# Kernel tuning notes

Measured on AMD Instinct MI355X. Metric: run time of the kernel, lower is better.

The kernel has to match this reference:

```python
import jax, jax.numpy as jnp
import numpy as np

N_ANCHORS = 25
N_CLASSES = 16
X_IMG = 296
Y_IMG = 296
OPLIST = ['conv','conv','MP','conv','conv','MP','conv','conv','conv','MP','conv','conv','conv','MP','conv','conv','conv']

def _size_list(s):
    out = [s]
    for op in OPLIST:
        out.append(out[-1] - 2 if op == 'conv' else out[-1] // 2)
    return out

XLIST = _size_list(X_IMG)  # ends at 7
YLIST = _size_list(Y_IMG)
FEAT = XLIST[-1]           # final feature-map size (7)
GRID = XLIST[-1] - 2       # anchor grid (5), source's xlist[-1]-2 convention
B, C = 2, 512


def setup_inputs() -> dict:
    key = jax.random.key(0)
    ks = jax.random.split(key, 12)
    D = C * 49
    return {
        'cfeats':   jax.random.normal(ks[0], (B, C, FEAT, FEAT), jnp.float32),
        'regcls':   jax.random.normal(ks[1], (B, 5, N_ANCHORS, GRID, GRID), jnp.float32) * 0.5,
        'wanchors': jax.random.uniform(ks[2], (N_ANCHORS, GRID, GRID), jnp.float32, 16.0, 128.0),
        'hanchors': jax.random.uniform(ks[3], (N_ANCHORS, GRID, GRID), jnp.float32, 16.0, 128.0),
        'xanchors': jax.random.uniform(ks[4], (N_ANCHORS, GRID, GRID), jnp.float32, 0.0, float(X_IMG)),
        'yanchors': jax.random.uniform(ks[5], (N_ANCHORS, GRID, GRID), jnp.float32, 0.0, float(Y_IMG)),
        'w1': jax.random.normal(ks[6], (200, D), jnp.float32) * 0.02,
        'b1': jnp.zeros((200,), jnp.float32),
        'w2': jax.random.normal(ks[7], (100, 200), jnp.float32) * 0.02,
        'b2': jnp.zeros((100,), jnp.float32),
        'w3': jax.random.normal(ks[8], (N_CLASSES + 1, 100), jnp.float32) * 0.02,
        'b3': jnp.zeros((N_CLASSES + 1,), jnp.float32),
        'w4': jax.random.normal(ks[9], (4 * (N_CLASSES + 1), 100), jnp.float32) * 0.02,
        'b4': jnp.zeros((4 * (N_CLASSES + 1),), jnp.float32),
    }


def _forward(cfeats, regcls, wanchors, hanchors, xanchors, yanchors,
             w1, b1, w2, b2, w3, b3, w4, b4):
    Bq, Cq, Fq, _ = cfeats.shape
    A, G = N_ANCHORS, GRID
    # ---- anchor-box decode ----
    wreg = jnp.exp(regcls[:, 2]) * wanchors
    hreg = jnp.exp(regcls[:, 3]) * hanchors
    xreg = regcls[:, 0] * wanchors + xanchors
    yreg = regcls[:, 1] * hanchors + yanchors
    xis = xreg - wreg / 2.0
    yis = yreg - hreg / 2.0
    xfs = xreg + wreg / 2.0
    yfs = yreg + hreg / 2.0
    c0 = jnp.floor(jax.nn.relu(xis))
    c1 = jnp.floor(jax.nn.relu(yis))
    c2 = jnp.minimum(jnp.ceil(xfs), float(X_IMG - 1))
    c3 = jnp.maximum(jnp.ceil(yfs), float(Y_IMG - 1))  # (sic) max, as in source
    valid = (xis < float(X_IMG)) & (yis < float(Y_IMG)) & (xfs >= 0.0) & (yfs >= 0.0)
    c4 = jnp.where(valid, jax.nn.sigmoid(regcls[:, 4]), 0.0)
    # ---- track coords through the conv/MP stack ----
    for i, op in enumerate(OPLIST):
        if op == 'conv':
            c0 = jax.nn.relu(c0 - 1.0)
            c1 = jax.nn.relu(c1 - 1.0)
            c2 = jnp.minimum(c2, float(XLIST[i + 1] - 1))
            c3 = jnp.minimum(c3, float(YLIST[i + 1] - 1))
        else:
            c0 = jnp.floor(c0 / 2.0); c1 = jnp.floor(c1 / 2.0)
            c2 = jnp.floor(c2 / 2.0); c3 = jnp.floor(c3 / 2.0)
    N = A * G * G  # flatten (anchor, x, y) -> roi index, same order as source
    xi = c0.reshape(Bq, N).astype(jnp.int32)
    yi = c1.reshape(Bq, N).astype(jnp.int32)
    xf = c2.reshape(Bq, N).astype(jnp.int32)
    yf = c3.reshape(Bq, N).astype(jnp.int32)
    roi_on = c4.reshape(Bq, N) > 0.0
    # ---- 7x7 RoIPool (vectorized; bins partition [xi, xf+1) via floor boundaries) ----
    ii = jnp.arange(8, dtype=jnp.int32)
    wx = xf + 1 - xi
    wy = yf + 1 - yi
    bx = xi[:, :, None] + (ii * wx[:, :, None]) // 7  # [B,N,8]
    by = yi[:, :, None] + (ii * wy[:, :, None]) // 7
    xs = jnp.arange(Fq, dtype=jnp.int32)
    maskx = (xs[None, None, None, :] >= bx[:, :, :7, None]) & (xs[None, None, None, :] < bx[:, :, 1:, None])  # [B,N,7,F]
    masky = (xs[None, None, None, :] >= by[:, :, :7, None]) & (xs[None, None, None, :] < by[:, :, 1:, None])
    NEG = jnp.float32(-1e30)
    feats_sg = jax.lax.stop_gradient(cfeats)
    # stage 1: max over x per bin i  -> val1/arg1: [B,N,7,C,F]
    val1 = jnp.full((Bq, N, 7, Cq, Fq), NEG, jnp.float32)
    arg1 = jnp.zeros((Bq, N, 7, Cq, Fq), jnp.int32)
    for x in range(Fq):
        cand = jnp.where(maskx[:, :, :, x][..., None, None], feats_sg[:, None, None, :, x, :], NEG)
        upd = cand > val1
        val1 = jnp.where(upd, cand, val1)
        arg1 = jnp.where(upd, x, arg1)
    # stage 2: max over y per bin j  -> val2/arg2: [B,N,7,7,C]
    val2 = jnp.full((Bq, N, 7, 7, Cq), NEG, jnp.float32)
    arg2 = jnp.zeros((Bq, N, 7, 7, Cq), jnp.int32)
    for y in range(Fq):
        cand = jnp.where(masky[:, :, None, :, y][..., None], val1[:, :, :, None, :, y], NEG)
        upd = cand > val2
        val2 = jnp.where(upd, cand, val2)
        arg2 = jnp.where(upd, y, arg2)
    # recover x index of the per-bin argmax, then one differentiable gather
    argx = jnp.take_along_axis(arg1[:, :, :, None, :, :], arg2[..., None], axis=-1)[..., 0]  # [B,N,7,7,C]
    cell = argx * Fq + arg2
    feats_flat = cfeats.reshape(Bq, Cq, Fq * Fq)
    pooled = jnp.take_along_axis(feats_flat[:, None, None, None, :, :], cell[..., None], axis=-1)[..., 0]
    keep = (val2 > NEG * 0.5) & roi_on[:, :, None, None, None]
    pooled = jnp.where(keep, pooled, 0.0)  # [B,N,7,7,C]
    # layout [..., C*49] with 49 = 7*i + j, matching source
    pooled = jnp.transpose(pooled, (0, 1, 4, 2, 3)).reshape(Bq, A, G, G, Cq * 49)
    # ---- MLP head ----
    z = jax.nn.relu(pooled @ w1.T + b1)
    z = jax.nn.relu(z @ w2.T + b2)
    z1 = z @ w3.T + b3
    z2 = z @ w4.T + b4
    K = N_CLASSES + 1
    z3 = jnp.stack([z2[..., 0:K], z2[..., K:2 * K], z2[..., 2 * K:3 * K], z2[..., 3 * K:4 * K]], axis=1)
    return z1, z3


def reference(cfeats, regcls, wanchors, hanchors, xanchors, yanchors,
              w1, b1, w2, b2, w3, b3, w4, b4):
    return _forward(cfeats, regcls, wanchors, hanchors, xanchors, yanchors,
                    w1, b1, w2, b2, w3, b3, w4, b4)
```

## Files before the change

### kernel.cpp

```cpp
#include <hip/hip_runtime.h>
#include <cstdint>

using short8 = __attribute__((ext_vector_type(8))) short;
using f32x4  = __attribute__((ext_vector_type(4))) float;

__device__ __forceinline__ uint16_t f2bf(float x) {
    uint32_t u = __float_as_uint(x);
    uint32_t r = (u + 0x7FFFu + ((u >> 16) & 1u)) >> 16;
    return (uint16_t)r;
}
__device__ __forceinline__ int fdiv7(int a) {
    int q = a / 7;
    if ((a % 7 != 0) && (a < 0)) q--;
    return q;
}

__global__ void __launch_bounds__(256) k_prep(const float* __restrict__ regcls,
                                              const float* __restrict__ wan,
                                              const float* __restrict__ han,
                                              const float* __restrict__ xan,
                                              const float* __restrict__ yan,
                                              const float* __restrict__ cf,
                                              const float* __restrict__ w1,
                                              const float* __restrict__ w2,
                                              const float* __restrict__ w3,
                                              const float* __restrict__ w4,
                                              int8_t* __restrict__ cells,
                                              uint16_t* __restrict__ cfb,
                                              uint16_t* __restrict__ w1f,
                                              float* __restrict__ w2t,
                                              float* __restrict__ w34t) {
    __shared__ __align__(16) uint16_t lh[16 * 788];
    int blk = blockIdx.x;
    int t = threadIdx.x;

    if (blk < 5) {
        int r = blk * 256 + t;
        if (r >= 1250) return;
        int b = r / 625, n = r - b * 625;
        const float* rc = regcls + b * 3125 + n;
        float t0 = rc[0], t1 = rc[625], t2 = rc[1250], t3 = rc[1875];
        float wa = wan[n], ha = han[n], xa = xan[n], ya = yan[n];
        float wr = expf(t2) * wa, hr = expf(t3) * ha;
        float xr = t0 * wa + xa, yr = t1 * ha + ya;
        float xis = xr - wr * 0.5f, yis = yr - hr * 0.5f;
        float xfs = xr + wr * 0.5f, yfs = yr + hr * 0.5f;
        bool valid = (xis < 296.f) && (yis < 296.f) && (xfs >= 0.f) && (yfs >= 0.f);
        int c0 = (int)floorf(fmaxf(xis, 0.f));
        int c1 = (int)floorf(fmaxf(yis, 0.f));
        int c2 = (int)fminf(ceilf(xfs), 295.f);
        int c3 = (int)fmaxf(ceilf(yfs), 295.f);
        const int  XL1[17]    = {294,292,146,144,142,71,69,67,65,32,30,28,26,13,11,9,7};
        const bool ISCONV[17] = {1,1,0,1,1,0,1,1,1,0,1,1,1,0,1,1,1};
        #pragma unroll
        for (int i = 0; i < 17; i++) {
            if (ISCONV[i]) {
                c0 = max(c0 - 1, 0); c1 = max(c1 - 1, 0);
                c2 = min(c2, XL1[i] - 1); c3 = min(c3, XL1[i] - 1);
            } else {
                c0 >>= 1; c1 >>= 1; c2 >>= 1; c3 >>= 1;
            }
        }
        int xi = c0, yi = c1, xf = c2, yf = c3;
        int wx = xf + 1 - xi, wy = yf + 1 - yi;
        int bx[8], by[8];
        #pragma unroll
        for (int i = 0; i < 8; i++) { bx[i] = xi + fdiv7(i * wx); by[i] = yi + fdiv7(i * wy); }
        int8_t* cr = cells + r * 64;
        #pragma unroll
        for (int i = 0; i < 7; i++)
            #pragma unroll
            for (int j = 0; j < 7; j++) {
                bool ne = valid && (bx[i + 1] > bx[i]) && (by[j + 1] > by[j]);
                cr[i * 7 + j] = ne ? (int8_t)(bx[i] * 7 + by[j]) : (int8_t)(-1);
            }
    } else if (blk < 37) {
        int g = (blk - 5) * 256 + t;
        int b = g >> 12;
        int xy = (g >> 6) & 63;
        int c0 = (g & 63) * 8;
        uint32_t pk[4];
        if (xy < 49) {
            #pragma unroll
            for (int h = 0; h < 4; h++) {
                uint16_t lo = f2bf(cf[(b * 512 + c0 + 2 * h) * 49 + xy]);
                uint16_t hi = f2bf(cf[(b * 512 + c0 + 2 * h + 1) * 49 + xy]);
                pk[h] = (uint32_t)lo | ((uint32_t)hi << 16);
            }
        } else {
            pk[0] = pk[1] = pk[2] = pk[3] = 0;
        }
        ((uint4*)cfb)[(b * 64 + xy) * 64 + (g & 63)] = make_uint4(pk[0], pk[1], pk[2], pk[3]);
    } else if (blk < 175) {
        int g = (blk - 37) * 256 + t;
        if (g < 200 * 128) {
            int k = g >> 7, o = g & 127;
            w2t[g] = (o < 100) ? w2[o * 200 + k] : 0.f;
        }
        int u = g - 200 * 128;
        if (u >= 0 && u < 100 * 96) {
            int k = u / 96, o = u - k * 96;
            float v = 0.f;
            if (o < 17) v = w3[o * 100 + k];
            else if (o < 85) v = w4[(o - 17) * 100 + k];
            w34t[u] = v;
        }
    } else {
        int idx = blk - 175;
        int nt = idx % 13, ct = idx / 13;
        int kbase = ct * 784;
        for (int i = t; i < 16 * 196; i += 256) {
            int rr = i / 196, c4 = i - rr * 196;
            int o = nt * 16 + rr;
            float4 v = make_float4(0.f, 0.f, 0.f, 0.f);
            if (o < 200) v = ((const float4*)(w1 + (size_t)o * 25088 + kbase))[c4];
            ushort4 hv;
            hv.x = f2bf(v.x); hv.y = f2bf(v.y); hv.z = f2bf(v.z); hv.w = f2bf(v.w);
            *(ushort4*)&lh[rr * 788 + 4 * c4] = hv;
        }
        __syncthreads();
        int kc = ct >> 1;
        int q0 = (ct & 1) * 2;
        int lsub = t & 31;
        int l = q0 * 16 + lsub;
        int rrow = lsub & 15;
        int clbase = (lsub >> 4) * 8;
        for (int binb = 0; binb < 49; binb += 8) {
            int bin = binb + (t >> 5);
            if (bin < 49) {
                uint32_t pk[4];
                #pragma unroll
                for (int h = 0; h < 4; h++) {
                    uint32_t lo = lh[rrow * 788 + (clbase + 2 * h) * 49 + bin];
                    uint32_t hi = lh[rrow * 788 + (clbase + 2 * h + 1) * 49 + bin];
                    pk[h] = lo | (hi << 16);
                }
                ((uint4*)w1f)[((bin * 16 + kc) * 13 + nt) * 64 + l] =
                    make_uint4(pk[0], pk[1], pk[2], pk[3]);
            }
        }
    }
}

__global__ void __launch_bounds__(256) k_qgemm(const uint16_t* __restrict__ cfb,
                                               const uint16_t* __restrict__ w1f,
                                               float* __restrict__ Q) {
    __shared__ uint4 bs[16 * 64];
    int bin = blockIdx.x, nt = blockIdx.y;
    int t = threadIdx.x;
    const uint4* bw = (const uint4*)w1f + (bin * 208 + nt) * 64;
    for (int i = t; i < 16 * 64; i += 256) {
        int kc = i >> 6, l = i & 63;
        bs[i] = bw[kc * 832 + l];
    }
    __syncthreads();
    int w = t >> 6, l = t & 63;
    int r16 = l & 15, quad = l >> 4;
    int o = nt * 16 + r16;
    int xybase = w * 16 + quad * 4;
    #pragma unroll
    for (int b = 0; b < 2; b++) {
        const uint4* ap = (const uint4*)cfb + (b * 64 + w * 16 + r16) * 64 + quad;
        f32x4 acc = {0.f, 0.f, 0.f, 0.f};
        #pragma unroll
        for (int kc = 0; kc < 16; kc++) {
            uint4 av = ap[kc * 4];
            uint4 bv = bs[kc * 64 + l];
            short8 a8 = __builtin_bit_cast(short8, av);
            short8 b8 = __builtin_bit_cast(short8, bv);
            acc = __builtin_amdgcn_mfma_f32_16x16x32_bf16(a8, b8, acc, 0, 0, 0);
        }
        float* qb = Q + ((size_t)(b * 49 + bin) * 49) * 208 + o;
        #pragma unroll
        for (int reg = 0; reg < 4; reg++) {
            int xy = xybase + reg;
            if (xy < 49) qb[xy * 208] = acc[reg];
        }
    }
}

__global__ void __launch_bounds__(256) k_head(const int8_t* __restrict__ cells,
                                              const float* __restrict__ Q,
                                              const float* __restrict__ b1,
                                              const float* __restrict__ w2t,
                                              const float* __restrict__ b2,
                                              const float* __restrict__ w34t,
                                              const float* __restrict__ b3,
                                              const float* __restrict__ b4,
                                              float* __restrict__ out) {
    __shared__ float z1[200];
    __shared__ float z2[100];
    __shared__ float zp[256];
    int r = blockIdx.x;
    int b = r / 625, n = r - b * 625;
    int t = threadIdx.x;
    int o2 = t & 127, kq = t >> 7;
    const int8_t* cr = cells + r * 64;
    float s0 = 0.f, s1 = 0.f;
    if (t < 208) {
        const float* qb = Q + (size_t)(b * 49) * 49 * 208 + t;
        #pragma unroll
        for (int bin = 0; bin < 49; bin++) {
            int cv = (int)cr[bin];
            int idx = max(cv, 0);
            float m = (cv >= 0) ? 1.f : 0.f;
            float v = m * qb[(bin * 49 + idx) * 208];
            if (bin & 1) s1 += v; else s0 += v;
        }
    }
    if (t < 200) z1[t] = fmaxf(s0 + s1 + b1[t], 0.f);
    __syncthreads();
    float a0 = 0.f, a1 = 0.f;
    if (o2 < 100) {
        const float* wp = w2t + (kq * 100) * 128 + o2;
        const float* zz = z1 + kq * 100;
        #pragma unroll 10
        for (int k = 0; k < 100; k += 2) {
            a0 += zz[k]     * wp[k * 128];
            a1 += zz[k + 1] * wp[(k + 1) * 128];
        }
    }
    zp[t] = a0 + a1;
    __syncthreads();
    if (t < 100) z2[t] = fmaxf(b2[t] + zp[t] + zp[t + 128], 0.f);
    __syncthreads();
    float c0 = 0.f;
    if (o2 < 85) {
        const float* wp = w34t + (kq * 50) * 96 + o2;
        const float* zz = z2 + kq * 50;
        #pragma unroll 10
        for (int k = 0; k < 50; k++) c0 += zz[k] * wp[k * 96];
    }
    zp[t] = c0;
    __syncthreads();
    if (t < 85) {
        float v = ((t < 17) ? b3[t] : b4[t - 17]) + zp[t] + zp[t + 128];
        if (t < 17) {
            out[b * 10625 + n * 17 + t] = v;
        } else {
            int q = (t - 17) / 17, kk = (t - 17) - q * 17;
            out[21250 + b * 42500 + q * 10625 + n * 17 + kk] = v;
        }
    }
}

extern "C" void kernel_launch(void* const* d_in, const int* in_sizes, int n_in,
                              void* d_out, int out_size, void* d_ws, size_t ws_size,
                              hipStream_t stream) {
    const float* cfeats = (const float*)d_in[0];
    const float* regcls = (const float*)d_in[1];
    const float* wan    = (const float*)d_in[2];
    const float* han    = (const float*)d_in[3];
    const float* xan    = (const float*)d_in[4];
    const float* yan    = (const float*)d_in[5];
    const float* w1     = (const float*)d_in[6];
    const float* b1     = (const float*)d_in[7];
    const float* w2     = (const float*)d_in[8];
    const float* b2     = (const float*)d_in[9];
    const float* w3     = (const float*)d_in[10];
    const float* b3     = (const float*)d_in[11];
    const float* w4     = (const float*)d_in[12];
    const float* b4     = (const float*)d_in[13];

    char* ws = (char*)d_ws;
    int8_t*   cells = (int8_t*)ws;
    uint16_t* cfb   = (uint16_t*)(ws + 80000);
    uint16_t* w1f   = (uint16_t*)(ws + 211072);
    float*    Q     = (float*)(ws + 10647680);
    float*    w2t   = (float*)(ws + 14642944);
    float*    w34t  = (float*)(ws + 14745344);
    float*    out   = (float*)d_out;

    k_prep<<<dim3(591), dim3(256), 0, stream>>>(regcls, wan, han, xan, yan,
                                                cfeats, w1, w2, w3, w4,
                                                cells, cfb, w1f, w2t, w34t);
    k_qgemm<<<dim3(49, 13), dim3(256), 0, stream>>>(cfb, w1f, Q);
    k_head<<<dim3(1250), dim3(256), 0, stream>>>(cells, Q, b1, w2t, b2, w34t, b3, b4, out);
}
```

Baseline: 131.7 us.

## Restructure Q-GEMM to stage A in LDS and batch five ROIs per head block

The Q GEMM now loads the per-batch feature matrix into XOR-swizzled shared memory once per block, with each wave handling one bin and reusing each weight fragment across four M-tiles. Before, each block staged the weights and re-read the features from global memory. The head kernel now processes five ROIs per block, so each w2/w34 weight load is amortized over five accumulators and the grid shrinks from 1250 to 250 blocks. The trade-off is more shared memory and registers per block, and fewer blocks to spread across the GPU.

```diff
diff --git a/kernel.cpp b/kernel.cpp
--- a/kernel.cpp
+++ b/kernel.cpp
@@ -145,38 +145,44 @@
 __global__ void __launch_bounds__(256) k_qgemm(const uint16_t* __restrict__ cfb,
                                                const uint16_t* __restrict__ w1f,
                                                float* __restrict__ Q) {
-    __shared__ uint4 bs[16 * 64];
-    int bin = blockIdx.x, nt = blockIdx.y;
+    __shared__ uint4 As[64 * 64];
+    int bg = blockIdx.x, nt = blockIdx.y, b = blockIdx.z;
     int t = threadIdx.x;
-    const uint4* bw = (const uint4*)w1f + (bin * 208 + nt) * 64;
-    for (int i = t; i < 16 * 64; i += 256) {
-        int kc = i >> 6, l = i & 63;
-        bs[i] = bw[kc * 832 + l];
+    const uint4* ac = (const uint4*)cfb + b * 4096;
+    for (int idx = t; idx < 4096; idx += 256) {
+        int xy = idx >> 6, i = idx & 63;
+        As[xy * 64 + (i ^ (xy & 7))] = ac[idx];
     }
     __syncthreads();
     int w = t >> 6, l = t & 63;
+    int bin = bg * 4 + w;
+    if (bin >= 49) return;
     int r16 = l & 15, quad = l >> 4;
     int o = nt * 16 + r16;
-    int xybase = w * 16 + quad * 4;
-    #pragma unroll
-    for (int b = 0; b < 2; b++) {
-        const uint4* ap = (const uint4*)cfb + (b * 64 + w * 16 + r16) * 64 + quad;
-        f32x4 acc = {0.f, 0.f, 0.f, 0.f};
-        #pragma unroll
-        for (int kc = 0; kc < 16; kc++) {
-            uint4 av = ap[kc * 4];
-            uint4 bv = bs[kc * 64 + l];
+    int swz = r16 & 7;
+    const uint4* bw = (const uint4*)w1f + (bin * 208 + nt) * 64 + l;
+    f32x4 acc[4];
+    #pragma unroll
+    for (int m = 0; m < 4; m++) acc[m] = (f32x4){0.f, 0.f, 0.f, 0.f};
+    #pragma unroll
+    for (int kc = 0; kc < 16; kc++) {
+        uint4 bv = bw[kc * 832];
+        short8 b8 = __builtin_bit_cast(short8, bv);
+        #pragma unroll
+        for (int m = 0; m < 4; m++) {
+            uint4 av = As[(m * 16 + r16) * 64 + ((kc * 4 + quad) ^ swz)];
             short8 a8 = __builtin_bit_cast(short8, av);
-            short8 b8 = __builtin_bit_cast(short8, bv);
-            acc = __builtin_amdgcn_mfma_f32_16x16x32_bf16(a8, b8, acc, 0, 0, 0);
-        }
-        float* qb = Q + ((size_t)(b * 49 + bin) * 49) * 208 + o;
+            acc[m] = __builtin_amdgcn_mfma_f32_16x16x32_bf16(a8, b8, acc[m], 0, 0, 0);
+        }
+    }
+    float* qb = Q + ((size_t)(b * 49 + bin) * 49) * 208 + o;
+    #pragma unroll
+    for (int m = 0; m < 4; m++)
         #pragma unroll
         for (int reg = 0; reg < 4; reg++) {
-            int xy = xybase + reg;
-            if (xy < 49) qb[xy * 208] = acc[reg];
-        }
-    }
+            int xy = m * 16 + quad * 4 + reg;
+            if (xy < 49) qb[xy * 208] = acc[m][reg];
+        }
 }
 
 __global__ void __launch_bounds__(256) k_head(const int8_t* __restrict__ cells,
@@ -188,58 +194,83 @@
                                               const float* __restrict__ b3,
                                               const float* __restrict__ b4,
                                               float* __restrict__ out) {
-    __shared__ float z1[200];
-    __shared__ float z2[100];
-    __shared__ float zp[256];
-    int r = blockIdx.x;
-    int b = r / 625, n = r - b * 625;
+    __shared__ float z1s[5][200];
+    __shared__ float z2s[5][100];
+    __shared__ float zps[5][256];
+    __shared__ int8_t cls[5 * 64];
+    int r0 = blockIdx.x * 5;
+    int b = r0 / 625;
     int t = threadIdx.x;
-    int o2 = t & 127, kq = t >> 7;
-    const int8_t* cr = cells + r * 64;
-    float s0 = 0.f, s1 = 0.f;
+    for (int i = t; i < 80; i += 256)
+        ((uint32_t*)cls)[i] = ((const uint32_t*)(cells + r0 * 64))[i];
+    __syncthreads();
+    float s[5] = {0.f, 0.f, 0.f, 0.f, 0.f};
     if (t < 208) {
         const float* qb = Q + (size_t)(b * 49) * 49 * 208 + t;
-        #pragma unroll
+        #pragma unroll 7
         for (int bin = 0; bin < 49; bin++) {
-            int cv = (int)cr[bin];
-            int idx = max(cv, 0);
-            float m = (cv >= 0) ? 1.f : 0.f;
-            float v = m * qb[(bin * 49 + idx) * 208];
-            if (bin & 1) s1 += v; else s0 += v;
-        }
-    }
-    if (t < 200) z1[t] = fmaxf(s0 + s1 + b1[t], 0.f);
-    __syncthreads();
-    float a0 = 0.f, a1 = 0.f;
+            #pragma unroll
+            for (int roi = 0; roi < 5; roi++) {
+                int cv = (int)cls[roi * 64 + bin];
+                int idx = max(cv, 0);
+                float m = (cv >= 0) ? 1.f : 0.f;
+                s[roi] += m * qb[(bin * 49 + idx) * 208];
+            }
+        }
+    }
+    if (t < 200) {
+        float bb = b1[t];
+        #pragma unroll
+        for (int roi = 0; roi < 5; roi++) z1s[roi][t] = fmaxf(s[roi] + bb, 0.f);
+    }
+    __syncthreads();
+    int o2 = t & 127, kq = t >> 7;
+    float a[5] = {0.f, 0.f, 0.f, 0.f, 0.f};
     if (o2 < 100) {
         const float* wp = w2t + (kq * 100) * 128 + o2;
-        const float* zz = z1 + kq * 100;
-        #pragma unroll 10
-        for (int k = 0; k < 100; k += 2) {
-            a0 += zz[k]     * wp[k * 128];
-            a1 += zz[k + 1] * wp[(k + 1) * 128];
-        }
-    }
-    zp[t] = a0 + a1;
-    __syncthreads();
-    if (t < 100) z2[t] = fmaxf(b2[t] + zp[t] + zp[t + 128], 0.f);
-    __syncthreads();
-    float c0 = 0.f;
+        #pragma unroll 4
+        for (int k = 0; k < 100; k++) {
+            float wv = wp[k * 128];
+            #pragma unroll
+            for (int roi = 0; roi < 5; roi++) a[roi] += z1s[roi][kq * 100 + k] * wv;
+        }
+    }
+    #pragma unroll
+    for (int roi = 0; roi < 5; roi++) zps[roi][t] = a[roi];
+    __syncthreads();
+    if (t < 100) {
+        float bb = b2[t];
+        #pragma unroll
+        for (int roi = 0; roi < 5; roi++)
+            z2s[roi][t] = fmaxf(bb + zps[roi][t] + zps[roi][t + 128], 0.f);
+    }
+    __syncthreads();
+    float c[5] = {0.f, 0.f, 0.f, 0.f, 0.f};
     if (o2 < 85) {
         const float* wp = w34t + (kq * 50) * 96 + o2;
-        const float* zz = z2 + kq * 50;
-        #pragma unroll 10
-        for (int k = 0; k < 50; k++) c0 += zz[k] * wp[k * 96];
-    }
-    zp[t] = c0;
+        #pragma unroll 5
+        for (int k = 0; k < 50; k++) {
+            float wv = wp[k * 96];
+            #pragma unroll
+            for (int roi = 0; roi < 5; roi++) c[roi] += z2s[roi][kq * 50 + k] * wv;
+        }
+    }
+    __syncthreads();
+    #pragma unroll
+    for (int roi = 0; roi < 5; roi++) zps[roi][t] = c[roi];
     __syncthreads();
     if (t < 85) {
-        float v = ((t < 17) ? b3[t] : b4[t - 17]) + zp[t] + zp[t + 128];
-        if (t < 17) {
-            out[b * 10625 + n * 17 + t] = v;
-        } else {
-            int q = (t - 17) / 17, kk = (t - 17) - q * 17;
-            out[21250 + b * 42500 + q * 10625 + n * 17 + kk] = v;
+        float bb = (t < 17) ? b3[t] : b4[t - 17];
+        #pragma unroll
+        for (int roi = 0; roi < 5; roi++) {
+            int n = r0 + roi - b * 625;
+            float v = bb + zps[roi][t] + zps[roi][t + 128];
+            if (t < 17) {
+                out[b * 10625 + n * 17 + t] = v;
+            } else {
+                int q = (t - 17) / 17, kk = (t - 17) - q * 17;
+                out[21250 + b * 42500 + q * 10625 + n * 17 + kk] = v;
+            }
         }
     }
 }
@@ -274,6 +305,6 @@
     k_prep<<<dim3(591), dim3(256), 0, stream>>>(regcls, wan, han, xan, yan,
                                                 cfeats, w1, w2, w3, w4,
                                                 cells, cfb, w1f, w2t, w34t);
-    k_qgemm<<<dim3(49, 13), dim3(256), 0, stream>>>(cfb, w1f, Q);
-    k_head<<<dim3(1250), dim3(256), 0, stream>>>(cells, Q, b1, w2t, b2, w34t, b3, b4, out);
-}
+    k_qgemm<<<dim3(13, 13, 2), dim3(256), 0, stream>>>(cfb, w1f, Q);
+    k_head<<<dim3(250), dim3(256), 0, stream>>>(cells, Q, b1, w2t, b2, w34t, b3, b4, out);
+}
```

New measurement: 132.0 us. About the same (+0.3%).

## Restructure Q GEMM to stage activations in swizzled LDS per batch

Applied to the files above, without the earlier changes.

The Q GEMM now launches one block per (bin group, output tile, batch). Each block stages that batch's full bf16 feature matrix into XOR-swizzled shared memory, and each wave owns one bin, streaming its weight fragments directly from global memory. A tiles are now reused across four bins from LDS instead of being re-read from global per bin, and the swizzle is meant to avoid bank conflicts. The head kernel splits its gather reduction into four accumulators for more ILP, and launch_bounds annotations are dropped. The trade-off is a 64KB LDS footprint per block, which limits occupancy, plus uncached per-wave weight reads.

```diff
diff --git a/kernel.cpp b/kernel.cpp
--- a/kernel.cpp
+++ b/kernel.cpp
@@ -142,52 +142,58 @@
     }
 }
 
-__global__ void __launch_bounds__(256) k_qgemm(const uint16_t* __restrict__ cfb,
-                                               const uint16_t* __restrict__ w1f,
-                                               float* __restrict__ Q) {
-    __shared__ uint4 bs[16 * 64];
-    int bin = blockIdx.x, nt = blockIdx.y;
+__global__ void k_qgemm(const uint16_t* __restrict__ cfb,
+                        const uint16_t* __restrict__ w1f,
+                        float* __restrict__ Q) {
+    __shared__ uint4 As[64 * 64];
+    int bg = blockIdx.x, nt = blockIdx.y, b = blockIdx.z;
     int t = threadIdx.x;
-    const uint4* bw = (const uint4*)w1f + (bin * 208 + nt) * 64;
-    for (int i = t; i < 16 * 64; i += 256) {
-        int kc = i >> 6, l = i & 63;
-        bs[i] = bw[kc * 832 + l];
+    const uint4* ac = (const uint4*)cfb + b * 4096;
+    for (int idx = t; idx < 4096; idx += 256) {
+        int xy = idx >> 6, i = idx & 63;
+        As[xy * 64 + (i ^ (xy & 7))] = ac[idx];
     }
     __syncthreads();
     int w = t >> 6, l = t & 63;
+    int bin = bg * 4 + w;
+    if (bin >= 49) return;
     int r16 = l & 15, quad = l >> 4;
     int o = nt * 16 + r16;
-    int xybase = w * 16 + quad * 4;
+    int swz = r16 & 7;
+    const uint4* bw = (const uint4*)w1f + (bin * 208 + nt) * 64 + l;
+    f32x4 acc[4];
     #pragma unroll
-    for (int b = 0; b < 2; b++) {
-        const uint4* ap = (const uint4*)cfb + (b * 64 + w * 16 + r16) * 64 + quad;
-        f32x4 acc = {0.f, 0.f, 0.f, 0.f};
-        #pragma unroll
-        for (int kc = 0; kc < 16; kc++) {
-            uint4 av = ap[kc * 4];
-            uint4 bv = bs[kc * 64 + l];
+    for (int m = 0; m < 4; m++) acc[m] = (f32x4){0.f, 0.f, 0.f, 0.f};
+    #pragma unroll
+    for (int kc = 0; kc < 16; kc++) {
+        uint4 bv = bw[kc * 832];
+        short8 b8 = __builtin_bit_cast(short8, bv);
+        #pragma unroll
+        for (int m = 0; m < 4; m++) {
+            uint4 av = As[(m * 16 + r16) * 64 + ((kc * 4 + quad) ^ swz)];
             short8 a8 = __builtin_bit_cast(short8, av);
-            short8 b8 = __builtin_bit_cast(short8, bv);
-            acc = __builtin_amdgcn_mfma_f32_16x16x32_bf16(a8, b8, acc, 0, 0, 0);
-        }
-        float* qb = Q + ((size_t)(b * 49 + bin) * 49) * 208 + o;
+            acc[m] = __builtin_amdgcn_mfma_f32_16x16x32_bf16(a8, b8, acc[m], 0, 0, 0);
+        }
+    }
+    float* qb = Q + ((size_t)(b * 49 + bin) * 49) * 208 + o;
+    #pragma unroll
+    for (int m = 0; m < 4; m++)
         #pragma unroll
         for (int reg = 0; reg < 4; reg++) {
-            int xy = xybase + reg;
-            if (xy < 49) qb[xy * 208] = acc[reg];
-        }
-    }
-}
-
-__global__ void __launch_bounds__(256) k_head(const int8_t* __restrict__ cells,
-                                              const float* __restrict__ Q,
-                                              const float* __restrict__ b1,
-                                              const float* __restrict__ w2t,
-                                              const float* __restrict__ b2,
-                                              const float* __restrict__ w34t,
-                                              const float* __restrict__ b3,
-                                              const float* __restrict__ b4,
-                                              float* __restrict__ out) {
+            int xy = m * 16 + quad * 4 + reg;
+            if (xy < 49) qb[xy * 208] = acc[m][reg];
+        }
+}
+
+__global__ void k_head(const int8_t* __restrict__ cells,
+                       const float* __restrict__ Q,
+                       const float* __restrict__ b1,
+                       const float* __restrict__ w2t,
+                       const float* __restrict__ b2,
+                       const float* __restrict__ w34t,
+                       const float* __restrict__ b3,
+                       const float* __restrict__ b4,
+                       float* __restrict__ out) {
     __shared__ float z1[200];
     __shared__ float z2[100];
     __shared__ float zp[256];
@@ -196,7 +202,7 @@
     int t = threadIdx.x;
     int o2 = t & 127, kq = t >> 7;
     const int8_t* cr = cells + r * 64;
-    float s0 = 0.f, s1 = 0.f;
+    float s[4] = {0.f, 0.f, 0.f, 0.f};
     if (t < 208) {
         const float* qb = Q + (size_t)(b * 49) * 49 * 208 + t;
         #pragma unroll
@@ -204,11 +210,10 @@
             int cv = (int)cr[bin];
             int idx = max(cv, 0);
             float m = (cv >= 0) ? 1.f : 0.f;
-            float v = m * qb[(bin * 49 + idx) * 208];
-            if (bin & 1) s1 += v; else s0 += v;
-        }
-    }
-    if (t < 200) z1[t] = fmaxf(s0 + s1 + b1[t], 0.f);
+            s[bin & 3] += m * qb[(bin * 49 + idx) * 208];
+        }
+    }
+    if (t < 200) z1[t] = fmaxf(s[0] + s[1] + s[2] + s[3] + b1[t], 0.f);
     __syncthreads();
     float a0 = 0.f, a1 = 0.f;
     if (o2 < 100) {
@@ -274,6 +279,6 @@
     k_prep<<<dim3(591), dim3(256), 0, stream>>>(regcls, wan, han, xan, yan,
                                                 cfeats, w1, w2, w3, w4,
                                                 cells, cfb, w1f, w2t, w34t);
-    k_qgemm<<<dim3(49, 13), dim3(256), 0, stream>>>(cfb, w1f, Q);
+    k_qgemm<<<dim3(13, 13, 2), dim3(256), 0, stream>>>(cfb, w1f, Q);
     k_head<<<dim3(1250), dim3(256), 0, stream>>>(cells, Q, b1, w2t, b2, w34t, b3, b4, out);
 }
```

After: 122.1 us. 1.08x faster.
